# Optimization experiments

Hardware: AMD Instinct MI355X
Metric: run time of the kernel (lower is better)

## Reference

```python
import jax, jax.numpy as jnp
import numpy as np

# ContextualAttention config (matches init_kwargs)
KS, STRIDE, DIL, FUSE_K, SCALE = 3, 1, 1, 3, 10.0
B, C, H, W = 2, 128, 64, 64
L = H * W  # number of background patches (SAME padding, stride 1)


def _same_pad(x, k, s):
    # TF-style SAME padding, identical to the repo's same_padding helper
    _, _, h, w = x.shape
    oh, ow = -(-h // s), -(-w // s)
    ph = max(0, (oh - 1) * s + k - h)
    pw = max(0, (ow - 1) * s + k - w)
    return jnp.pad(x, ((0, 0), (0, 0), (ph // 2, ph - ph // 2), (pw // 2, pw - pw // 2)))


def _patches(x, k, s):
    # extract_image_patches: SAME pad + unfold -> [N, L, C*k*k], (c, kh, kw) ordering
    xp = _same_pad(x, k, s)
    n, c, hp, wp = xp.shape
    oh, ow = (hp - k) // s + 1, (wp - k) // s + 1
    cols = jnp.stack(
        [xp[:, :, i:i + (oh - 1) * s + 1:s, j:j + (ow - 1) * s + 1:s]
         for i in range(k) for j in range(k)], axis=2)  # [N, C, k*k, oh, ow]
    return cols.reshape(n, c * k * k, oh * ow).transpose(0, 2, 1)


def _fuse(scores):
    # diagonal fuse-smoothing: conv the [L_b, L_f] score matrix with eye(k), twice
    # (second pass on the transposed spatial layout), exactly as in the torch code
    bn = scores.shape[0]
    eye = jnp.eye(FUSE_K, dtype=scores.dtype)[None, None]  # [1,1,k,k]
    conv = lambda v: jax.lax.conv_general_dilated(
        v, eye, (1, 1), [(1, 1), (1, 1)],
        dimension_numbers=('NCHW', 'OIHW', 'NCHW'))
    y = conv(scores.reshape(bn, 1, L, L))
    y = y.reshape(bn, H, W, H, W).transpose(0, 2, 1, 4, 3).reshape(bn, 1, L, L)
    y = conv(y)
    y = y.reshape(bn, W, H, W, H).transpose(0, 2, 1, 4, 3)  # back to [b,H,W,H,W]
    return y.reshape(bn, L, H, W)


def setup_inputs() -> dict:
    key = jax.random.key(0)
    kf, kb, km = jax.random.split(key, 3)
    f = jax.random.normal(kf, (B, C, H, W), jnp.float32)
    b = jax.random.normal(kb, (B, C, H, W), jnp.float32)
    mask = (jax.random.uniform(km, (1, 1, H, W)) < 0.05).astype(jnp.float32)
    return {"f": f, "b": b, "mask": mask}


def reference(f, b, mask):
    kernel = 2 * DIL  # raw patch size for aggregation (=2)
    # raw background patches used by the transposed-conv aggregation
    raw_w = _patches(b, kernel, DIL * STRIDE).reshape(B, L, C, kernel, kernel)
    # DIL == 1 => F.interpolate(scale=1.0, nearest) is identity on f/b/mask
    w = _patches(b, KS, STRIDE)      # [B, L, C*9] matching patches
    fp = _patches(f, KS, 1)          # [B, Lf, C*9] foreground patches (SAME pad)
    m = _patches(mask, KS, STRIDE)[0]                    # [L, 9]
    mm = (jnp.mean(m, axis=1) == 0.0).astype(f.dtype)    # [L] 1 = patch usable

    # per-patch L2 normalization (clamped at 1e-4), conv-as-similarity == patch GEMM
    wn = w / jnp.maximum(jnp.sqrt(jnp.sum(w * w, axis=2, keepdims=True)), 1e-4)
    scores = jnp.einsum('bkd,bqd->bkq', wn, fp).reshape(B, L, H, W)
    scores = _fuse(scores)

    mmb = mm[None, :, None, None]
    attn = jax.nn.softmax(scores * mmb * SCALE, axis=1) * mmb  # softmax over L

    # conv_transpose2d(attn, raw_w, stride=1, padding=1) == VALID corr with flipped,
    # IO-swapped 2x2 kernel (k-1-p = 0 padding); per-sample weights -> vmap
    def agg(a, rw):  # a: [L,H,W], rw: [L,C,2,2]
        rhs = jnp.flip(rw, axis=(2, 3)).transpose(1, 0, 2, 3)  # [C, L, 2, 2] OIHW
        return jax.lax.conv_general_dilated(
            a[None], rhs, (1, 1), [(0, 0), (0, 0)],
            dimension_numbers=('NCHW', 'OIHW', 'NCHW'))[0]

    y = jax.vmap(agg)(attn, raw_w) / 4.0       # [B, C, H-1, W-1]
    y = jnp.pad(y, ((0, 0), (0, 0), (0, 1), (0, 1)))  # output_padding = DIL % 2 = 1
    return y
```

## Files before the change

### kernel.cpp

```cpp
#include <hip/hip_runtime.h>

#define L 4096
#define HH 64
#define CC 128
#define BB 2

typedef _Float16 f16;
typedef _Float16 f16x8 __attribute__((ext_vector_type(8)));
typedef float f32x4 __attribute__((ext_vector_type(4)));

__device__ __forceinline__ void gl_lds16(const f16* g, f16* l) {
  __builtin_amdgcn_global_load_lds(
      (const __attribute__((address_space(1))) void*)g,
      (__attribute__((address_space(3))) void*)l, 16, 0, 0);
}

__device__ __forceinline__ int sigma_(int j) { return ((j & 63) << 6) | (j >> 6); }

__device__ float fuse9(const f16* __restrict__ Sb, int k, int j) {
  float acc = 0.f;
  int cK = sigma_(k), cQ = sigma_(j);
#pragma unroll
  for (int u = -1; u <= 1; ++u) {
    int a = cK + u, bq = cQ + u;
    if ((unsigned)a < L && (unsigned)bq < L) {
      int r = sigma_(a), c = sigma_(bq);
#pragma unroll
      for (int t = -1; t <= 1; ++t) {
        int rr = r + t, cc = c + t;
        if ((unsigned)rr < L && (unsigned)cc < L) acc += (float)Sb[(size_t)rr * L + cc];
      }
    }
  }
  return acc;
}

__global__ __launch_bounds__(256) void k_repack(
    const float* __restrict__ b, const float* __restrict__ f,
    f16* __restrict__ bT, f16* __restrict__ fT, f16* __restrict__ zp,
    float* __restrict__ ssq) {
  __shared__ float tile[128][65];
  __shared__ float ss[4][64];
  int u0 = blockIdx.x * 64;
  int z = blockIdx.y;
  int batch = z >> 1;
  const float* src = ((z & 1) ? f : b) + (size_t)batch * CC * L;
  f16* dst = ((z & 1) ? fT : bT) + (size_t)batch * L * CC;
  int tid = threadIdx.x;
  if (blockIdx.x == 0 && z == 0 && tid < 32) zp[tid] = (f16)0.f;
#pragma unroll
  for (int i = 0; i < 32; ++i) {
    int idx = i * 256 + tid;
    int c = idx >> 6, ux = idx & 63;
    tile[c][ux] = src[(size_t)c * L + u0 + ux];
  }
  __syncthreads();
  if (!(z & 1)) {
    int ux = tid & 63, prt = tid >> 6;
    float s = 0.f;
#pragma unroll 8
    for (int c = prt * 32; c < prt * 32 + 32; ++c) { float v = tile[c][ux]; s += v * v; }
    ss[prt][ux] = s;
  }
#pragma unroll
  for (int j = 0; j < 4; ++j) {
    int t2 = j * 256 + tid;
    int u = t2 >> 4, ch = t2 & 15;
    f16x8 v;
#pragma unroll
    for (int e = 0; e < 8; ++e) v[e] = (f16)tile[ch * 8 + e][u];
    *(f16x8*)(dst + (size_t)(u0 + u) * CC + ch * 8) = v;
  }
  __syncthreads();
  if (!(z & 1) && tid < 64)
    ssq[batch * L + u0 + tid] = ss[0][tid] + ss[1][tid] + ss[2][tid] + ss[3][tid];
}

__global__ void k_norm(const float* __restrict__ ssq, float* __restrict__ inv_n) {
  int gi = blockIdx.x * 256 + threadIdx.x;
  if (gi >= BB * L) return;
  int batch = gi >> 12, k = gi & (L - 1);
  int ky = k >> 6, kx = k & 63;
  float s = 0.f;
#pragma unroll
  for (int dy = -1; dy <= 1; ++dy)
#pragma unroll
    for (int dx = -1; dx <= 1; ++dx) {
      if ((unsigned)(ky + dy) < 64 && (unsigned)(kx + dx) < 64)
        s += ssq[batch * L + k + dy * 64 + dx];
    }
  inv_n[gi] = 1.f / fmaxf(sqrtf(s), 1e-4f);
}

__global__ __launch_bounds__(256) void k_prep_bm(const float* __restrict__ b, f16* __restrict__ bm) {
  int idx = blockIdx.x * 256 + threadIdx.x;
  int e8 = idx * 8;
  int k0 = e8 & (L - 1);
  int c = (e8 >> 12) & (CC - 1);
  int bt = e8 >> 19;
  int batch = bt & 1;
  int tap = bt >> 1;
  int di = 1 - (tap >> 1), dj = 1 - (tap & 1);
  int ky = k0 >> 6, kx0 = k0 & 63;
  const float* src = b + ((size_t)batch * CC + c) * L + k0 + di * 64 + dj;
  bool rowok = (ky + di) < 64;
  f16x8 v;
#pragma unroll
  for (int e = 0; e < 8; ++e) {
    float x = (rowok && (kx0 + e + dj) < 64) ? src[e] : 0.f;
    v[e] = (f16)x;
  }
  *(f16x8*)(bm + (size_t)e8) = v;
}

__global__ void k_prep_mm(const float* __restrict__ mask, float* __restrict__ mmv,
                          float* __restrict__ zcnt) {
  __shared__ float sm[256];
  int tid = threadIdx.x;
  int k = blockIdx.x * 256 + tid;
  int ky = k >> 6, kx = k & 63;
  float s = 0.f;
  for (int i = 0; i < 3; ++i)
    for (int j = 0; j < 3; ++j) {
      int yy = ky + i - 1, xx = kx + j - 1;
      if (yy >= 0 && yy < 64 && xx >= 0 && xx < 64) s += mask[yy * 64 + xx];
    }
  float v = (s == 0.f) ? 1.f : 0.f;
  mmv[k] = v;
  sm[tid] = v;
  __syncthreads();
  if (tid < 32) {
    float c = 0.f;
#pragma unroll
    for (int r = 0; r < 8; ++r) c += (sm[tid * 8 + r] == 0.f) ? 1.f : 0.f;
    zcnt[blockIdx.x * 32 + tid] = c;
  }
}

__global__ __launch_bounds__(256) void k_gemm_scores(
    const f16* __restrict__ bT, const f16* __restrict__ fT,
    const float* __restrict__ inv_n, const f16* __restrict__ zp,
    f16* __restrict__ S) {
  __shared__ f16 As[2][128 * 64];
  __shared__ f16 Bs[2][128 * 64];
  int qt = blockIdx.x, kt = blockIdx.y, batch = blockIdx.z;
  int tid = threadIdx.x, wid = tid >> 6, lane = tid & 63;
  int wr = wid >> 1, wc = wid & 1;
  const f16* A0 = bT + (size_t)batch * L * CC;
  const f16* B0 = fT + (size_t)batch * L * CC;
  f32x4 acc[4][4] = {};
  int rA = wr * 64 + (lane & 15);
  int rB = wc * 64 + (lane & 15);

  const f16* baseA_[4]; const f16* baseB_[4];
  int offL_[4];
  unsigned mA_[4], mB_[4];
#pragma unroll
  for (int i = 0; i < 4; ++i) {
    int chunk = (i * 4 + wid) * 64 + lane;
    int row = chunk >> 3;
    int lg = (lane & 7) ^ (row & 7);
    int k = kt * 128 + row;
    int q = qt * 128 + row;
    baseA_[i] = A0 + (size_t)k * CC + lg * 8;
    baseB_[i] = B0 + (size_t)q * CC + lg * 8;
    offL_[i] = chunk * 8;
    int ky = k >> 6, kx = k & 63, qy = q >> 6, qx = q & 63;
    unsigned ma = 0, mb = 0;
#pragma unroll
    for (int rr = 0; rr < 9; ++rr) {
      int dy = rr / 3 - 1, dx = rr - (rr / 3) * 3 - 1;
      if ((unsigned)(ky + dy) < 64u && (unsigned)(kx + dx) < 64u) ma |= 1u << rr;
      if ((unsigned)(qy + dy) < 64u && (unsigned)(qx + dx) < 64u) mb |= 1u << rr;
    }
    mA_[i] = ma; mB_[i] = mb;
  }

#define STAGE_T(tt, bsel)                                                     \
  do {                                                                        \
    int rr_ = (tt) >> 1, half_ = (tt) & 1;                                    \
    int dy_ = rr_ / 3 - 1, dx_ = rr_ - (rr_ / 3) * 3 - 1;                     \
    int doff_ = (dy_ * 64 + dx_) * CC + half_ * 64;                           \
    _Pragma("unroll")                                                         \
    for (int i = 0; i < 4; ++i) {                                             \
      gl_lds16(((mA_[i] >> rr_) & 1u) ? (baseA_[i] + doff_) : zp,             \
               &As[bsel][0] + offL_[i]);                                      \
      gl_lds16(((mB_[i] >> rr_) & 1u) ? (baseB_[i] + doff_) : zp,             \
               &Bs[bsel][0] + offL_[i]);                                      \
    }                                                                         \
  } while (0)

  STAGE_T(0, 0);
  int cur = 0;
#pragma unroll 1
  for (int t = 0; t < 18; ++t) {
    __syncthreads();
    if (t < 17) STAGE_T(t + 1, cur ^ 1);
    const f16* Ab = &As[cur][0];
    const f16* Bb = &Bs[cur][0];
#pragma unroll
    for (int h2 = 0; h2 < 2; ++h2) {
      int cb = h2 * 4 + (lane >> 4);
      f16x8 af[4], bf[4];
#pragma unroll
      for (int m = 0; m < 4; ++m) {
        int row = rA + m * 16;
        af[m] = *(const f16x8*)(Ab + row * 64 + ((cb ^ (row & 7)) * 8));
      }
#pragma unroll
      for (int n = 0; n < 4; ++n) {
        int row = rB + n * 16;
        bf[n] = *(const f16x8*)(Bb + row * 64 + ((cb ^ (row & 7)) * 8));
      }
#pragma unroll
      for (int m = 0; m < 4; ++m)
#pragma unroll
        for (int n = 0; n < 4; ++n)
          acc[m][n] = __builtin_amdgcn_mfma_f32_16x16x32_f16(af[m], bf[n], acc[m][n], 0, 0, 0);
    }
    cur ^= 1;
  }
#undef STAGE_T

  f16* Srow = S + (size_t)batch * L * L;
  int kbase = kt * 128 + wr * 64 + (lane >> 4) * 4;
  int qbase = qt * 128 + wc * 64 + (lane & 15);
#pragma unroll
  for (int m = 0; m < 4; ++m) {
    f32x4 invv = *(const f32x4*)(inv_n + (size_t)batch * L + kbase + m * 16);
#pragma unroll
    for (int r = 0; r < 4; ++r) {
      f16* dst = Srow + (size_t)(kbase + m * 16 + r) * L + qbase;
#pragma unroll
      for (int n = 0; n < 4; ++n) dst[n * 16] = (f16)(acc[m][n][r] * invv[r]);
    }
  }
}

__global__ __launch_bounds__(256) void k_fuse_stats(
    const f16* __restrict__ S, const float* __restrict__ mmv,
    f16* __restrict__ PT, float* __restrict__ pmP, float* __restrict__ pl) {
  int tid = threadIdx.x;
  int wave = tid >> 6, lane = tid & 63;
  int g = blockIdx.x * 64 + lane;
  if (g >= 494) return;
  int kb = blockIdx.y, batch = blockIdx.z;
  int q0 = 72 + g * 8;
  int k0 = kb * 32 + wave * 8;
  const f16* Sb = S + (size_t)batch * L * L;
  f16* Pb = PT + (size_t)batch * L * L;
  float lg[8][8];
  float m8[8];
#pragma unroll
  for (int e = 0; e < 8; ++e) m8[e] = -3.0e38f;
  unsigned vmask = 0;
#pragma unroll
  for (int kk = 0; kk < 8; ++kk) {
    int k = k0 + kk;
    if (mmv[k] == 0.f) continue;
    vmask |= 1u << kk;
    float acc[8] = {0.f, 0.f, 0.f, 0.f, 0.f, 0.f, 0.f, 0.f};
    int cK = sigma_(k);
#pragma unroll
    for (int u = -1; u <= 1; ++u) {
      int a = cK + u;
      if ((unsigned)a >= L) continue;
      int r = sigma_(a);
      const f16* cb = Sb + (size_t)r * L + (q0 + 64 * u);
      {
        f16x8 v = *(const f16x8*)cb;
#pragma unroll
        for (int e = 0; e < 8; ++e) acc[e] += (float)v[e];
      }
      if (r >= 1) {
        const f16* rm = cb - L;
        f16x8 v = *(const f16x8*)rm;
        acc[0] += (float)rm[-1];
#pragma unroll
        for (int e = 1; e < 8; ++e) acc[e] += (float)v[e - 1];
      }
      if (r <= L - 2) {
        const f16* rp = cb + L;
        f16x8 v = *(const f16x8*)rp;
#pragma unroll
        for (int e = 0; e < 7; ++e) acc[e] += (float)v[e + 1];
        acc[7] += (float)rp[8];
      }
    }
#pragma unroll
    for (int e = 0; e < 8; ++e) {
      float x = acc[e] * 10.f;
      lg[kk][e] = x;
      m8[e] = fmaxf(m8[e], x);
    }
  }
  float l8[8] = {0.f, 0.f, 0.f, 0.f, 0.f, 0.f, 0.f, 0.f};
#pragma unroll
  for (int kk = 0; kk < 8; ++kk) {
    if ((vmask >> kk) & 1u) {
#pragma unroll
      for (int e = 0; e < 8; ++e) {
        float p = __expf(lg[kk][e] - m8[e]);
        l8[e] += p;
        lg[kk][e] = p;
      }
    } else {
#pragma unroll
      for (int e = 0; e < 8; ++e) lg[kk][e] = 0.f;
    }
  }
#pragma unroll
  for (int e = 0; e < 8; ++e) {
    f16 v[8];
#pragma unroll
    for (int kk = 0; kk < 8; ++kk) v[kk] = (f16)lg[kk][e];
    *(f16x8*)(Pb + (size_t)(q0 + e) * L + k0) = *(f16x8*)v;
  }
  int ck = kb * 4 + wave;
  float* pmp = pmP + (size_t)ck * (BB * L) + (size_t)batch * L + q0;
  float* plp = pl + (size_t)ck * (BB * L) + (size_t)batch * L + q0;
  *(f32x4*)pmp = *(f32x4*)&m8[0]; *(f32x4*)(pmp + 4) = *(f32x4*)&m8[4];
  *(f32x4*)plp = *(f32x4*)&l8[0]; *(f32x4*)(plp + 4) = *(f32x4*)&l8[4];
}

__global__ __launch_bounds__(256) void k_fuse_stats_edge(
    const f16* __restrict__ S, const float* __restrict__ mmv,
    f16* __restrict__ PT, float* __restrict__ pmP, float* __restrict__ pl) {
  int tid = threadIdx.x;
  if (tid >= 144) return;
  int q = (tid < 72) ? tid : (4024 + tid - 72);
  int ck = blockIdx.x, batch = blockIdx.y;
  int k0 = ck * 8;
  const f16* Sb = S + (size_t)batch * L * L;
  f16* Pb = PT + (size_t)batch * L * L;
  float lgs[8];
  float m = -3.0e38f;
  unsigned vmask = 0;
#pragma unroll
  for (int kk = 0; kk < 8; ++kk) {
    int k = k0 + kk;
    if (mmv[k] == 0.f) continue;
    vmask |= 1u << kk;
    float x = 10.f * fuse9(Sb, k, q);
    lgs[kk] = x;
    m = fmaxf(m, x);
  }
  float l = 0.f;
  f16 v[8];
#pragma unroll
  for (int kk = 0; kk < 8; ++kk) {
    if ((vmask >> kk) & 1u) {
      float p = __expf(lgs[kk] - m);
      l += p;
      v[kk] = (f16)p;
    } else {
      v[kk] = (f16)0.f;
    }
  }
  *(f16x8*)(Pb + (size_t)q * L + k0) = *(f16x8*)v;
  pmP[(size_t)ck * (BB * L) + (size_t)batch * L + q] = m;
  pl[(size_t)ck * (BB * L) + (size_t)batch * L + q] = l;
}

__global__ __launch_bounds__(256) void k_softmax_reduce(
    const float* __restrict__ pmP, const float* __restrict__ pl,
    const float* __restrict__ zcnt,
    float* __restrict__ Mq, float* __restrict__ invLq) {
  __shared__ float sm[4][64], sl[4][64];
  int tid = threadIdx.x;
  int ql = tid & 63, part = tid >> 6;
  int qi = blockIdx.x * 64 + ql;
  float m = -3.0e38f, l = 0.f;
  int i0 = part * 128;
  float cntp = 0.f;
#pragma unroll 4
  for (int i = i0; i < i0 + 128; ++i) {
    float pmv = pmP[(size_t)i * (BB * L) + qi];
    float plv = pl[(size_t)i * (BB * L) + qi];
    float nm = fmaxf(m, pmv);
    l = l * __expf(m - nm) + plv * __expf(pmv - nm);
    m = nm;
    cntp += zcnt[i & 511];
  }
  if (cntp > 0.f) {
    float nm = fmaxf(m, 0.f);
    l = l * __expf(m - nm) + cntp * __expf(-nm);
    m = nm;
  }
  sm[part][ql] = m; sl[part][ql] = l;
  __syncthreads();
  if (part == 0) {
    float M = sm[0][ql];
#pragma unroll
    for (int p = 1; p < 4; ++p) M = fmaxf(M, sm[p][ql]);
    float Ls = 0.f;
#pragma unroll
    for (int p = 0; p < 4; ++p) Ls += sl[p][ql] * __expf(sm[p][ql] - M);
    Mq[qi] = M;
    invLq[qi] = 1.f / Ls;
  }
}

__global__ __launch_bounds__(512) void k_agg(
    const f16* __restrict__ PT, const float* __restrict__ pmP,
    const float* __restrict__ Mq, const float* __restrict__ invLq,
    const f16* __restrict__ bm, float* __restrict__ part) {
  __shared__ f16 Asm[512 * 32];
  __shared__ f16 Bt[136 * 40];
  int pt = blockIdx.x, ks = blockIdx.y, batch = blockIdx.z;
  int p0 = pt * 64;
  int tid = threadIdx.x, wid = tid >> 6, lane = tid & 63;
  int wr = wid >> 1, wc = wid & 1;
  const f16* Pb = PT + (size_t)batch * L * L;

  const f16* gA_[4]; f16* lA_[4];
#pragma unroll
  for (int i = 0; i < 4; ++i) {
    int R = wid * 64 + i * 16 + (lane >> 2);
    int tap = R >> 7, c = R & 127;
    int chl = (lane & 3) ^ ((R >> 1) & 3);
    gA_[i] = bm + (((size_t)(tap * 2 + batch) * CC + c) * L) + chl * 8;
    lA_[i] = Asm + R * 32 + (lane & 3) * 8;
  }

  bool act1 = (tid < 32);
  int kg_[2]; bool qok_[2]; float M_[2], iL_[2];
  const f16* ptb_[2]; f16* bw_[2];
  size_t bq_[2];
#pragma unroll
  for (int s = 0; s < 2; ++s) {
    int tau = tid + s * 512;
    int kgv = tau & 3, ppv = tau >> 2;
    if (tau >= 544) { ppv = 0; kgv = 0; }
    kg_[s] = kgv;
    int q = p0 + ppv;
    bool qok = q < L;
    int qc = qok ? q : (L - 1);
    qok_[s] = qok;
    M_[s] = Mq[(size_t)batch * L + qc];
    iL_[s] = invLq[(size_t)batch * L + qc];
    ptb_[s] = Pb + (size_t)qc * L + kgv * 8;
    bq_[s] = (size_t)batch * L + qc;
    bw_[s] = Bt + ppv * 40 + ((kgv ^ ((ppv >> 3) & 3)) * 8);
  }

  f16x8 vv_[2];
  int kend = ks * 512 + 512;

#define LOADB(K0)                                                             \
  do {                                                                        \
    _Pragma("unroll")                                                         \
    for (int s = 0; s < 2; ++s) {                                             \
      if (s == 1 && !act1) break;                                             \
      f16x8 pv = *(const f16x8*)(ptb_[s] + (K0));                             \
      int ck = ((K0) >> 3) + kg_[s];                                          \
      float pmv = pmP[(size_t)ck * (BB * L) + bq_[s]];                        \
      float corr = qok_[s] ? __expf(pmv - M_[s]) * iL_[s] : 0.f;              \
      f16 v[8];                                                               \
      _Pragma("unroll")                                                       \
      for (int j = 0; j < 8; ++j) v[j] = (f16)((float)pv[j] * corr);          \
      vv_[s] = *(f16x8*)v;                                                    \
    }                                                                         \
  } while (0)

  LOADB(ks * 512);
  f32x4 acc[2][2] = {};
#pragma unroll 1
  for (int k0 = ks * 512; k0 < kend; k0 += 32) {
    __syncthreads();
    *(f16x8*)bw_[0] = vv_[0];
    if (act1) *(f16x8*)bw_[1] = vv_[1];
#pragma unroll
    for (int i = 0; i < 4; ++i) gl_lds16(gA_[i] + k0, lA_[i]);
    __syncthreads();
#pragma unroll
    for (int tap = 0; tap < 4; ++tap) {
      int dlt = (tap >> 1) * 64 + (tap & 1);
      f16x8 af[2], bf[2];
#pragma unroll
      for (int m = 0; m < 2; ++m) {
        int R = tap * 128 + wr * 32 + m * 16 + (lane & 15);
        int ph = (lane >> 4) ^ ((R >> 1) & 3);
        af[m] = *(const f16x8*)(Asm + R * 32 + ph * 8);
      }
#pragma unroll
      for (int n = 0; n < 2; ++n) {
        int pp = wc * 32 + n * 16 + (lane & 15) + dlt;
        int ph = (lane >> 4) ^ ((pp >> 3) & 3);
        bf[n] = *(const f16x8*)(Bt + pp * 40 + ph * 8);
      }
#pragma unroll
      for (int m = 0; m < 2; ++m)
#pragma unroll
        for (int n = 0; n < 2; ++n)
          acc[m][n] = __builtin_amdgcn_mfma_f32_16x16x32_f16(af[m], bf[n], acc[m][n], 0, 0, 0);
    }
    if (k0 + 32 < kend) LOADB(k0 + 32);
  }
#undef LOADB

  int cb = wr * 32 + (lane >> 4) * 4;
  int pb = p0 + wc * 32 + (lane & 15);
#pragma unroll
  for (int m = 0; m < 2; ++m)
#pragma unroll
    for (int n = 0; n < 2; ++n)
#pragma unroll
      for (int r = 0; r < 4; ++r) {
        int c = cb + m * 16 + r;
        int p = pb + n * 16;
        part[(((size_t)ks * 2 + batch) * CC + c) * L + p] = acc[m][n][r];
      }
}

__global__ __launch_bounds__(256) void k_agg_reduce(const float* __restrict__ part, float* __restrict__ out) {
  int idx = (blockIdx.x * 256 + threadIdx.x) * 4;
  f32x4 s = {0.f, 0.f, 0.f, 0.f};
#pragma unroll
  for (int ks = 0; ks < 8; ++ks) {
    f32x4 v = *(const f32x4*)(part + (size_t)ks * (2 * CC * L) + idx);
#pragma unroll
    for (int e = 0; e < 4; ++e) s[e] += v[e];
  }
  int p = idx & (L - 1);
  int u = p >> 6, vv = p & 63;
  f32x4 o;
#pragma unroll
  for (int e = 0; e < 4; ++e) o[e] = (u < 63 && (vv + e) < 63) ? s[e] * 0.25f : 0.f;
  *(f32x4*)(out + idx) = o;
}

extern "C" void kernel_launch(void* const* d_in, const int* in_sizes, int n_in,
                              void* d_out, int out_size, void* d_ws, size_t ws_size,
                              hipStream_t stream) {
  const float* f = (const float*)d_in[0];
  const float* b = (const float*)d_in[1];
  const float* mask = (const float*)d_in[2];
  float* out = (float*)d_out;
  char* ws = (char*)d_ws;

  f16* PT    = (f16*)(ws + 0);
  f16* S     = (f16*)(ws + 67108864);
  f16* bm    = (f16*)(ws + 134217728);
  float* pmP = (float*)(ws + 142606336);
  float* pl  = (float*)(ws + 159383552);
  float* part= (float*)(ws + 176160768);
  float* mmv = (float*)(ws + 209715200);
  float* Mq  = (float*)(ws + 209731584);
  float* iLq = (float*)(ws + 209764352);
  f16* bT    = (f16*)(ws + 209797120);
  f16* fT    = (f16*)(ws + 211894272);
  float* ssq = (float*)(ws + 213991424);
  float* invn= (float*)(ws + 214024192);
  f16* zp    = (f16*)(ws + 214056960);
  float* zcnt= (float*)(ws + 214057088);

  k_repack<<<dim3(64, 4), dim3(256), 0, stream>>>(b, f, bT, fT, zp, ssq);
  k_norm<<<dim3(32), dim3(256), 0, stream>>>(ssq, invn);
  k_prep_bm<<<dim3(2048), dim3(256), 0, stream>>>(b, bm);
  k_prep_mm<<<dim3(16), dim3(256), 0, stream>>>(mask, mmv, zcnt);
  k_gemm_scores<<<dim3(32, 32, 2), dim3(256), 0, stream>>>(bT, fT, invn, zp, S);
  k_fuse_stats<<<dim3(8, 128, 2), dim3(256), 0, stream>>>(S, mmv, PT, pmP, pl);
  k_fuse_stats_edge<<<dim3(512, 2), dim3(256), 0, stream>>>(S, mmv, PT, pmP, pl);
  k_softmax_reduce<<<dim3(128), dim3(256), 0, stream>>>(pmP, pl, zcnt, Mq, iLq);
  k_agg<<<dim3(64, 8, 2), dim3(512), 0, stream>>>(PT, pmP, Mq, iLq, bm, part);
  k_agg_reduce<<<dim3(1024), dim3(256), 0, stream>>>(part, out);
}
```

Measured before the change: 317.2 us.

## Split GEMM reduction dimension across wave pairs with LDS partial-sum reduce

The score GEMM's warp tiling changes from a 2x2 output split to a 2-way output-row split combined with a 2-way split of the K chunk. Each wave now computes a 64x128 tile over half of each 64-wide K slice, and the two halves are summed through LDS in the epilogue. This halves the B-fragment LDS reads per wave relative to the MFMA count and removes the inner h2 loop. In exchange, accumulator registers double (128 floats), which risks lower occupancy or spills, and the epilogue gains an LDS reduction step with two extra barriers.

```diff
diff --git a/kernel.cpp b/kernel.cpp
--- a/kernel.cpp
+++ b/kernel.cpp
@@ -145,12 +145,13 @@
   __shared__ f16 Bs[2][128 * 64];
   int qt = blockIdx.x, kt = blockIdx.y, batch = blockIdx.z;
   int tid = threadIdx.x, wid = tid >> 6, lane = tid & 63;
-  int wr = wid >> 1, wc = wid & 1;
+  int wr = wid >> 1, h = wid & 1;
   const f16* A0 = bT + (size_t)batch * L * CC;
   const f16* B0 = fT + (size_t)batch * L * CC;
-  f32x4 acc[4][4] = {};
+  f32x4 acc[4][8] = {};
   int rA = wr * 64 + (lane & 15);
-  int rB = wc * 64 + (lane & 15);
+  int rB = lane & 15;
+  int cb = h * 4 + (lane >> 4);
 
   const f16* baseA_[4]; const f16* baseB_[4];
   int offL_[4];
@@ -198,41 +199,54 @@
     if (t < 17) STAGE_T(t + 1, cur ^ 1);
     const f16* Ab = &As[cur][0];
     const f16* Bb = &Bs[cur][0];
-#pragma unroll
-    for (int h2 = 0; h2 < 2; ++h2) {
-      int cb = h2 * 4 + (lane >> 4);
-      f16x8 af[4], bf[4];
-#pragma unroll
-      for (int m = 0; m < 4; ++m) {
-        int row = rA + m * 16;
-        af[m] = *(const f16x8*)(Ab + row * 64 + ((cb ^ (row & 7)) * 8));
-      }
-#pragma unroll
-      for (int n = 0; n < 4; ++n) {
-        int row = rB + n * 16;
-        bf[n] = *(const f16x8*)(Bb + row * 64 + ((cb ^ (row & 7)) * 8));
-      }
+    f16x8 af[4];
+#pragma unroll
+    for (int m = 0; m < 4; ++m) {
+      int row = rA + m * 16;
+      af[m] = *(const f16x8*)(Ab + row * 64 + ((cb ^ (row & 7)) * 8));
+    }
+#pragma unroll
+    for (int n = 0; n < 8; ++n) {
+      int row = rB + n * 16;
+      f16x8 bf = *(const f16x8*)(Bb + row * 64 + ((cb ^ (row & 7)) * 8));
 #pragma unroll
       for (int m = 0; m < 4; ++m)
-#pragma unroll
-        for (int n = 0; n < 4; ++n)
-          acc[m][n] = __builtin_amdgcn_mfma_f32_16x16x32_f16(af[m], bf[n], acc[m][n], 0, 0, 0);
+        acc[m][n] = __builtin_amdgcn_mfma_f32_16x16x32_f16(af[m], bf, acc[m][n], 0, 0, 0);
     }
     cur ^= 1;
   }
 #undef STAGE_T
 
-  f16* Srow = S + (size_t)batch * L * L;
-  int kbase = kt * 128 + wr * 64 + (lane >> 4) * 4;
-  int qbase = qt * 128 + wc * 64 + (lane & 15);
-#pragma unroll
-  for (int m = 0; m < 4; ++m) {
-    f32x4 invv = *(const f32x4*)(inv_n + (size_t)batch * L + kbase + m * 16);
-#pragma unroll
-    for (int r = 0; r < 4; ++r) {
-      f16* dst = Srow + (size_t)(kbase + m * 16 + r) * L + qbase;
-#pragma unroll
-      for (int n = 0; n < 4; ++n) dst[n * 16] = (f16)(acc[m][n][r] * invv[r]);
+  __syncthreads();
+  float* red = (wr == 0) ? (float*)&As[0][0] : (float*)&Bs[0][0];
+  int rloc = (lane >> 4) * 4;
+  int cloc = lane & 15;
+  if (h == 1) {
+#pragma unroll
+    for (int m = 0; m < 4; ++m)
+#pragma unroll
+      for (int n = 0; n < 8; ++n)
+#pragma unroll
+        for (int r = 0; r < 4; ++r)
+          red[(m * 16 + rloc + r) * 128 + n * 16 + cloc] = acc[m][n][r];
+  }
+  __syncthreads();
+  if (h == 0) {
+    f16* Srow = S + (size_t)batch * L * L;
+    int kbase = kt * 128 + wr * 64 + rloc;
+    int qbase = qt * 128 + cloc;
+#pragma unroll
+    for (int m = 0; m < 4; ++m) {
+      f32x4 invv = *(const f32x4*)(inv_n + (size_t)batch * L + kbase + m * 16);
+#pragma unroll
+      for (int r = 0; r < 4; ++r) {
+        f16* dst = Srow + (size_t)(kbase + m * 16 + r) * L + qbase;
+#pragma unroll
+        for (int n = 0; n < 8; ++n) {
+          float v = acc[m][n][r] + red[(m * 16 + rloc + r) * 128 + n * 16 + cloc];
+          dst[n * 16] = (f16)(v * invv[r]);
+        }
+      }
     }
   }
 }
```

Measured after the change: 401.2 us. 1.26x slower.
